# Kernel optimization log

Hardware: AMD Instinct MI355X
Metric: run time of the kernel (lower is better)

## Reference

```python
import jax, jax.numpy as jnp
import numpy as np

B, L, D, H = 2, 2048, 1024, 16
DH = D // H  # 64
SIGMA = float(np.sqrt(DH))  # sigma=None, learnable_sigma=False -> sqrt(d_head)


def setup_inputs() -> dict:
    key = jax.random.key(0)
    ks = jax.random.split(key, 5)
    x = jax.random.normal(ks[0], (B, L, D), dtype=jnp.float32)
    # causal visibility mask (1 = visible, 0 = masked), [B,1,L,L]
    mask = jnp.broadcast_to(jnp.tril(jnp.ones((L, L), jnp.int32))[None, None], (B, 1, L, L))
    scale = 0.02
    W_q = jax.random.normal(ks[1], (D, D), dtype=jnp.float32) * scale
    W_k = jax.random.normal(ks[2], (D, D), dtype=jnp.float32) * scale
    W_v = jax.random.normal(ks[3], (D, D), dtype=jnp.float32) * scale
    W_o = jax.random.normal(ks[4], (D, D), dtype=jnp.float32) * scale
    return {"x": x, "mask": mask, "W_q": W_q, "W_k": W_k, "W_v": W_v, "W_o": W_o}


def _split_heads(t):
    # [B,L,D] -> [B,H,L,DH]
    b, l, _ = t.shape
    return t.reshape(b, l, H, DH).transpose(0, 2, 1, 3)


def reference(x, mask, W_q, W_k, W_v, W_o):
    # nn.Linear(bias=False): y = x @ W.T
    Qh = _split_heads(x @ W_q.T)  # [B,H,L,DH]
    Kh = _split_heads(x @ W_k.T)
    Vh = _split_heads(x @ W_v.T)
    # RBF scores: -||q-k||^2 / (2 sigma^2)
    q_norm2 = jnp.sum(Qh * Qh, axis=-1, keepdims=True)          # [B,H,L,1]
    k_norm2 = jnp.sum(Kh * Kh, axis=-1)[..., None, :]            # [B,H,1,L]
    dot_qk = jnp.einsum('bhqd,bhkd->bhqk', Qh, Kh)               # [B,H,L,L]
    dist2 = q_norm2 + k_norm2 - 2.0 * dot_qk
    scores = -dist2 / (2.0 * SIGMA * SIGMA)
    scores = jnp.where(mask == 0, -jnp.inf, scores)
    attn = jax.nn.softmax(scores, axis=-1)
    Oh = jnp.einsum('bhqk,bhkd->bhqd', attn, Vh)                 # [B,H,L,DH]
    O = Oh.transpose(0, 2, 1, 3).reshape(B, L, D)
    return O @ W_o.T
```

## Files before the change

### kernel.cpp

```cpp
#include <hip/hip_runtime.h>

#define L_SEQ  2048
#define D_MODEL 1024
#define NH 16
#define DHEAD 64
#define BATCH 2

typedef __attribute__((ext_vector_type(8))) short bf16x8;
typedef __attribute__((ext_vector_type(4))) float f32x4;

__device__ inline ushort f2bf(float f) {
  unsigned int u = __builtin_bit_cast(unsigned int, f);
  return (ushort)((u + 0x7FFFu + ((u >> 16) & 1u)) >> 16);
}
__device__ inline float bf2f(ushort u) {
  return __builtin_bit_cast(float, (unsigned int)u << 16);
}

__device__ __forceinline__ void gload_lds16(const void* g, void* l) {
  __builtin_amdgcn_global_load_lds(
      (const __attribute__((address_space(1))) void*)g,
      (__attribute__((address_space(3))) void*)l, 16, 0, 0);
}

#define PROJ8 524288
#define WSZ8  131072
__global__ __launch_bounds__(256) void cvt_all(const float* __restrict__ x,
                                               const float* __restrict__ w0,
                                               const float* __restrict__ w1,
                                               const float* __restrict__ w2,
                                               const float* __restrict__ w3,
                                               ushort* __restrict__ xb,
                                               ushort* __restrict__ ob0,
                                               ushort* __restrict__ ob1,
                                               ushort* __restrict__ ob2,
                                               ushort* __restrict__ ob3) {
  const int gid = blockIdx.x * 256 + threadIdx.x;
  const float* in; ushort* out; int off;
  if (gid < PROJ8) { in = x; out = xb; off = gid; }
  else {
    const int j = gid - PROJ8;
    const int seg = j / WSZ8;
    off = j - seg * WSZ8;
    switch (seg) {
      case 0: in = w0; out = ob0; break;
      case 1: in = w1; out = ob1; break;
      case 2: in = w2; out = ob2; break;
      default: in = w3; out = ob3; break;
    }
  }
  const float4* p = (const float4*)in + (size_t)off * 2;
  const float4 a = p[0], b = p[1];
  ushort4 lo, hi;
  lo.x = f2bf(a.x); lo.y = f2bf(a.y); lo.z = f2bf(a.z); lo.w = f2bf(a.w);
  hi.x = f2bf(b.x); hi.y = f2bf(b.y); hi.z = f2bf(b.z); hi.w = f2bf(b.w);
  ((ushort4*)out)[(size_t)off * 2] = lo;
  ((ushort4*)out)[(size_t)off * 2 + 1] = hi;
}

__global__ __launch_bounds__(256) void gemm128(const ushort* __restrict__ A,
    const ushort* __restrict__ W0, const ushort* __restrict__ W1,
    const ushort* __restrict__ W2, ushort* __restrict__ o0,
    ushort* __restrict__ o1, ushort* __restrict__ o2,
    float* __restrict__ of, int fused) {
  __shared__ ushort As[2][128][32];
  __shared__ ushort Bs[2][128][32];
  const int tid = threadIdx.x;
  const int w = tid >> 6, l = tid & 63, lr = l & 15, lg = l >> 4;
  const int wr = w >> 1, wc = w & 1;

  const int cpx = gridDim.x >> 3;
  const int swz = (blockIdx.x & 7) * cpx + (blockIdx.x >> 3);
  const int NX = fused ? 24 : 8;
  const int ntile = swz % NX;
  const int m0 = (swz / NX) * 128;

  const ushort* W; ushort* ob; int mode;
  if (fused) {
    if (ntile < 8)       { W = W0; ob = o0; mode = 1; }
    else if (ntile < 16) { W = W1; ob = o1; mode = 1; }
    else                 { W = W2; ob = o2; mode = 2; }
  } else { W = W0; ob = o0; mode = 0; }
  const int n0 = (ntile & 7) * 128;

  const int srow = tid >> 2;
  const int skc_sw = (tid & 3) ^ (srow & 3);
  const ushort* Ag = A + (size_t)(m0 + srow) * D_MODEL + skc_sw * 8;
  const ushort* Wg = W + (size_t)(n0 + srow) * D_MODEL + skc_sw * 8;

#define STAGE(buf, k0)                                                      \
  {                                                                         \
    gload_lds16(Ag + (k0), &As[buf][0][0] + tid * 8);                       \
    gload_lds16(Ag + (size_t)64 * D_MODEL + (k0), &As[buf][0][0] + 2048 + tid * 8); \
    gload_lds16(Wg + (k0), &Bs[buf][0][0] + tid * 8);                       \
    gload_lds16(Wg + (size_t)64 * D_MODEL + (k0), &Bs[buf][0][0] + 2048 + tid * 8); \
  }

  STAGE(0, 0);

  f32x4 acc[4][4] = {};
  const int NT = D_MODEL / 32;
  for (int t = 0; t < NT; ++t) {
    const int cur = t & 1;
    if (t + 1 < NT) {
      STAGE(cur ^ 1, (t + 1) * 32);
      asm volatile("s_waitcnt vmcnt(4)" ::: "memory");
    } else {
      asm volatile("s_waitcnt vmcnt(0)" ::: "memory");
    }
    __builtin_amdgcn_s_barrier();

    bf16x8 af[4], bfv[4];
#pragma unroll
    for (int i = 0; i < 4; ++i)
      af[i] = *(const bf16x8*)&As[cur][wr * 64 + i * 16 + lr][(lg ^ (lr & 3)) * 8];
#pragma unroll
    for (int j = 0; j < 4; ++j)
      bfv[j] = *(const bf16x8*)&Bs[cur][wc * 64 + j * 16 + lr][(lg ^ (lr & 3)) * 8];
#pragma unroll
    for (int i = 0; i < 4; ++i)
#pragma unroll
      for (int j = 0; j < 4; ++j)
        acc[i][j] = __builtin_amdgcn_mfma_f32_16x16x32_bf16(af[i], bfv[j], acc[i][j], 0, 0, 0);
    __syncthreads();
  }

  if (mode == 0) {
#pragma unroll
    for (int i = 0; i < 4; ++i)
#pragma unroll
      for (int r = 0; r < 4; ++r) {
        const int m = m0 + wr * 64 + i * 16 + lg * 4 + r;
#pragma unroll
        for (int j = 0; j < 4; ++j)
          of[(size_t)m * D_MODEL + n0 + wc * 64 + j * 16 + lr] = acc[i][j][r];
      }
  } else if (mode == 1) {
    const int h = (ntile & 7) * 2 + wc;
#pragma unroll
    for (int i = 0; i < 4; ++i)
#pragma unroll
      for (int r = 0; r < 4; ++r) {
        const int m = m0 + wr * 64 + i * 16 + lg * 4 + r;
        const int b = m >> 11, ll = m & (L_SEQ - 1);
#pragma unroll
        for (int j = 0; j < 4; ++j)
          ob[((size_t)(b * NH + h) * L_SEQ + ll) * DHEAD + j * 16 + lr] = f2bf(acc[i][j][r]);
      }
  } else {
    const int h = (ntile & 7) * 2 + wc;
#pragma unroll
    for (int i = 0; i < 4; ++i) {
      const int mb = m0 + wr * 64 + i * 16 + lg * 4;
      const int b = mb >> 11, ll = mb & (L_SEQ - 1);
#pragma unroll
      for (int j = 0; j < 4; ++j) {
        ushort4 v;
        v.x = f2bf(acc[i][j][0]); v.y = f2bf(acc[i][j][1]);
        v.z = f2bf(acc[i][j][2]); v.w = f2bf(acc[i][j][3]);
        *(ushort4*)(ob + ((size_t)(b * NH + h) * DHEAD + j * 16 + lr) * L_SEQ + ll) = v;
      }
    }
  }
#undef STAGE
}

__global__ __launch_bounds__(256) void kn_bf16(const ushort* __restrict__ K,
                                               float* __restrict__ Kn) {
  const int i = blockIdx.x * 256 + threadIdx.x;
  const ushort4* p = (const ushort4*)(K + (size_t)i * DHEAD);
  float s = 0.f;
#pragma unroll
  for (int j = 0; j < 16; ++j) {
    const ushort4 v = p[j];
    const float a = bf2f(v.x), b = bf2f(v.y), c = bf2f(v.z), d = bf2f(v.w);
    s += a * a + b * b + c * c + d * d;
  }
  Kn[i] = s * 0.0078125f;
}

__global__ __launch_bounds__(512, 4) void attn_mfma3(const ushort* __restrict__ Q,
                                                     const ushort* __restrict__ K,
                                                     const ushort* __restrict__ Vt,
                                                     const float* __restrict__ Kexp,
                                                     ushort* __restrict__ Ob) {
  const int blk = blockIdx.x;
  const int qb = 15 - (blk >> 5);
  const int bh = blk & 31;
  const int tid = threadIdx.x;
  const int w = tid >> 6, l = tid & 63, lr = l & 15, lg = l >> 4;
  const int q0w = qb * 128 + w * 16;
  const int nt = 2 * qb + 2;
  const int tbw = q0w >> 6;

  __shared__ ushort Ks[2][64][64];
  __shared__ ushort Vs[2][64][64];
  __shared__ ushort P[8][16][70];

  const size_t ho = (size_t)bh * L_SEQ * DHEAD;
  const ushort* Qh = Q + ho;
  const ushort* Kh = K + ho;
  const ushort* Vh = Vt + ho;
  const float* KeB = Kexp + (size_t)bh * L_SEQ;

  const bf16x8 qf0 = *(const bf16x8*)(Qh + (size_t)(q0w + lr) * DHEAD + lg * 8);
  const bf16x8 qf1 = *(const bf16x8*)(Qh + (size_t)(q0w + lr) * DHEAD + 32 + lg * 8);

  const int srow = tid >> 3;
  const int scs = (tid & 7) ^ (srow & 7);
  const ushort* Kg = Kh + (size_t)srow * DHEAD + scs * 8;
  const ushort* Vg = Vh + (size_t)srow * L_SEQ + scs * 8;

  gload_lds16(Kg, &Ks[0][0][0] + tid * 8);
  gload_lds16(Vg, &Vs[0][0][0] + tid * 8);

  f32x4 oacc[4] = {};
  f32x4 lsacc = {};
  bf16x8 ones;
#pragma unroll
  for (int i = 0; i < 8; ++i) ones[i] = (short)0x3F80;

  for (int t = 0; t < nt; ++t) {
    const int cur = t & 1;
    if (t + 1 < nt) {
      const size_t kb2 = (size_t)(t + 1) * 64;
      gload_lds16(Kg + kb2 * DHEAD, &Ks[cur ^ 1][0][0] + tid * 8);
      gload_lds16(Vg + kb2, &Vs[cur ^ 1][0][0] + tid * 8);
      asm volatile("s_waitcnt vmcnt(2)" ::: "memory");
    } else {
      asm volatile("s_waitcnt vmcnt(0)" ::: "memory");
    }
    __builtin_amdgcn_s_barrier();

    const int kbase = t * 64;
    float ke[4];
#pragma unroll
    for (int nf = 0; nf < 4; ++nf) ke[nf] = KeB[kbase + nf * 16 + lr];
    const bool maskT = (t >= tbw);

    __builtin_amdgcn_s_setprio(1);
#pragma unroll
    for (int nf = 0; nf < 4; ++nf) {
      const int row = nf * 16 + lr;
      const bf16x8 kf0 = *(const bf16x8*)&Ks[cur][row][((lg) ^ (lr & 7)) * 8];
      const bf16x8 kf1 = *(const bf16x8*)&Ks[cur][row][((4 + lg) ^ (lr & 7)) * 8];
      f32x4 s = {0.f, 0.f, 0.f, 0.f};
      s = __builtin_amdgcn_mfma_f32_16x16x32_bf16(qf0, kf0, s, 0, 0, 0);
      s = __builtin_amdgcn_mfma_f32_16x16x32_bf16(qf1, kf1, s, 0, 0, 0);
      const int key = kbase + row;
      const float keh = ke[nf];
#pragma unroll
      for (int r = 0; r < 4; ++r) {
        float p = __expf(s[r] * 0.015625f - keh);
        if (maskT && key > q0w + lg * 4 + r) p = 0.f;
        P[w][lg * 4 + r][nf * 16 + lr] = f2bf(p);
      }
    }
    const bf16x8 p0 = *(const bf16x8*)&P[w][lr][lg * 8];
    const bf16x8 p1 = *(const bf16x8*)&P[w][lr][32 + lg * 8];
    lsacc = __builtin_amdgcn_mfma_f32_16x16x32_bf16(p0, ones, lsacc, 0, 0, 0);
    lsacc = __builtin_amdgcn_mfma_f32_16x16x32_bf16(p1, ones, lsacc, 0, 0, 0);
#pragma unroll
    for (int nf = 0; nf < 4; ++nf) {
      const int row = nf * 16 + lr;
      const bf16x8 vf0 = *(const bf16x8*)&Vs[cur][row][((lg) ^ (lr & 7)) * 8];
      const bf16x8 vf1 = *(const bf16x8*)&Vs[cur][row][((4 + lg) ^ (lr & 7)) * 8];
      oacc[nf] = __builtin_amdgcn_mfma_f32_16x16x32_bf16(p0, vf0, oacc[nf], 0, 0, 0);
      oacc[nf] = __builtin_amdgcn_mfma_f32_16x16x32_bf16(p1, vf1, oacc[nf], 0, 0, 0);
    }
    __builtin_amdgcn_s_setprio(0);
    __syncthreads();
  }

  const int b = bh >> 4, h = bh & 15;
#pragma unroll
  for (int r = 0; r < 4; ++r) {
    const float inv = 1.0f / lsacc[r];
    const int q = q0w + lg * 4 + r;
#pragma unroll
    for (int nf = 0; nf < 4; ++nf)
      Ob[((size_t)(b * L_SEQ + q)) * D_MODEL + h * DHEAD + nf * 16 + lr] =
          f2bf(oacc[nf][r] * inv);
  }
}

extern "C" void kernel_launch(void* const* d_in, const int* in_sizes, int n_in,
                              void* d_out, int out_size, void* d_ws, size_t ws_size,
                              hipStream_t stream) {
  const float* x  = (const float*)d_in[0];
  const float* Wq = (const float*)d_in[2];
  const float* Wk = (const float*)d_in[3];
  const float* Wv = (const float*)d_in[4];
  const float* Wo = (const float*)d_in[5];

  const size_t PROJ = (size_t)BATCH * L_SEQ * D_MODEL;
  const size_t WSZ  = (size_t)D_MODEL * D_MODEL;
  ushort* xb  = (ushort*)d_ws;
  ushort* Wqb = xb + PROJ;
  ushort* Wkb = Wqb + WSZ;
  ushort* Wvb = Wkb + WSZ;
  ushort* Wob = Wvb + WSZ;
  ushort* Qb  = Wob + WSZ;
  ushort* Kb  = Qb + PROJ;
  ushort* Vtb = Kb + PROJ;
  ushort* Obf = Vtb + PROJ;
  float*  Kn  = (float*)(Obf + PROJ);

  cvt_all<<<(PROJ8 + 4 * WSZ8) / 256, 256, 0, stream>>>(x, Wq, Wk, Wv, Wo,
                                                        xb, Wqb, Wkb, Wvb, Wob);
  gemm128<<<768, 256, 0, stream>>>(xb, Wqb, Wkb, Wvb, Qb, Kb, Vtb, nullptr, 1);
  kn_bf16<<<BATCH * NH * L_SEQ / 256, 256, 0, stream>>>(Kb, Kn);
  attn_mfma3<<<BATCH * NH * (L_SEQ / 128), 512, 0, stream>>>(Qb, Kb, Vtb, Kn, Obf);
  gemm128<<<256, 256, 0, stream>>>(Obf, Wob, nullptr, nullptr, Obf, nullptr,
                                   nullptr, (float*)d_out, 0);
}
```

Measured before the change: 146.9 us.

## Replace QKV projection GEMM with 256x256-tile 8-wave phased pipeline kernel

Adds a new QKV projection kernel that uses 256x256 output tiles with 8 waves, K-steps of 64, and double-buffered LDS. Global-to-LDS loads are split across four compute phases so each MFMA phase overlaps one staging load, with setprio raised around the MFMA bursts. The larger tile raises arithmetic intensity per LDS byte, but the grid drops from 768 blocks to 192 on a 256-CU part, which risks underfilling the device. The output GEMM is simplified to a single mode, and one trailing __syncthreads in the attention loop becomes a raw s_barrier.

```diff
diff --git a/kernel.cpp b/kernel.cpp
--- a/kernel.cpp
+++ b/kernel.cpp
@@ -58,11 +58,149 @@
   ((ushort4*)out)[(size_t)off * 2 + 1] = hi;
 }
 
+__global__ __launch_bounds__(512, 2) void gemm8p(const ushort* __restrict__ A,
+    const ushort* __restrict__ W0, const ushort* __restrict__ W1,
+    const ushort* __restrict__ W2, ushort* __restrict__ Qb,
+    ushort* __restrict__ Kb, ushort* __restrict__ Vtb) {
+  __shared__ ushort As[2][2][128][64];
+  __shared__ ushort Bs[2][2][128][64];
+  const int tid = threadIdx.x;
+  const int wid = tid >> 6, l = tid & 63, lr = l & 15, lg = l >> 4;
+  const int wr = wid >> 2, wc = wid & 3;
+
+  const int bid = blockIdx.x;
+  const int swz = (bid & 7) * 24 + (bid >> 3);
+  const int mt = swz / 12, nt_ = swz % 12;
+  const int m0g = mt * 256;
+  const ushort* W = (nt_ < 4) ? W0 : (nt_ < 8) ? W1 : W2;
+  ushort* outQK = (nt_ < 4) ? Qb : Kb;
+  const int mode2 = (nt_ >= 8);
+  const int ncol0 = (nt_ & 3) * 256;
+
+  const int srow = tid >> 3;
+  const int schunk = (tid & 7) ^ (srow & 7);
+  const ushort* Ag = A + (size_t)(m0g + srow) * D_MODEL + schunk * 8;
+  const ushort* Wg = W + (size_t)(ncol0 + srow) * D_MODEL + schunk * 8;
+  ushort* AsL = &As[0][0][0][0] + tid * 8;
+  ushort* BsL = &Bs[0][0][0][0] + tid * 8;
+
+#define STG_A(sl, h, T2)                                                        \
+  {                                                                             \
+    gload_lds16(Ag + (size_t)((h) * 128) * D_MODEL + (T2) * 64,                 \
+                AsL + (sl) * 16384 + (h) * 8192);                               \
+    gload_lds16(Ag + (size_t)((h) * 128 + 64) * D_MODEL + (T2) * 64,            \
+                AsL + (sl) * 16384 + (h) * 8192 + 4096);                        \
+  }
+#define STG_B(sl, h, T2)                                                        \
+  {                                                                             \
+    gload_lds16(Wg + (size_t)((h) * 128) * D_MODEL + (T2) * 64,                 \
+                BsL + (sl) * 16384 + (h) * 8192);                               \
+    gload_lds16(Wg + (size_t)((h) * 128 + 64) * D_MODEL + (T2) * 64,            \
+                BsL + (sl) * 16384 + (h) * 8192 + 4096);                        \
+  }
+
+  STG_A(0, 0, 0); STG_A(0, 1, 0); STG_B(0, 0, 0); STG_B(0, 1, 0);
+
+  f32x4 acc[8][4] = {};
+  bf16x8 bfr[4][2];
+  const int NT = D_MODEL / 64;
+
+#define PHASE(q)                                                                \
+  {                                                                             \
+    bf16x8 af[2][2];                                                            \
+    _Pragma("unroll") for (int m2 = 0; m2 < 2; ++m2)                            \
+      _Pragma("unroll") for (int kk = 0; kk < 2; ++kk)                          \
+        af[m2][kk] = *(const bf16x8*)&As[s][wr][((q) * 2 + m2) * 16 + lr]       \
+                                           [((kk * 4 + lg) ^ (lr & 7)) * 8];    \
+    if (T + 1 < NT) {                                                           \
+      if ((q) == 1)      { STG_A(s ^ 1, 1, T + 1); }                            \
+      else if ((q) == 2) { STG_B(s ^ 1, 0, T + 1); }                            \
+      else               { STG_B(s ^ 1, 1, T + 1); }                            \
+    }                                                                           \
+    __builtin_amdgcn_s_barrier();                                               \
+    __builtin_amdgcn_s_setprio(1);                                              \
+    _Pragma("unroll") for (int m2 = 0; m2 < 2; ++m2)                            \
+      _Pragma("unroll") for (int kk = 0; kk < 2; ++kk)                          \
+        _Pragma("unroll") for (int n = 0; n < 4; ++n)                           \
+          acc[(q) * 2 + m2][n] = __builtin_amdgcn_mfma_f32_16x16x32_bf16(       \
+              af[m2][kk], bfr[n][kk], acc[(q) * 2 + m2][n], 0, 0, 0);           \
+    __builtin_amdgcn_s_setprio(0);                                              \
+    __builtin_amdgcn_s_barrier();                                               \
+  }
+
+  for (int T = 0; T < NT; ++T) {
+    const int s = T & 1;
+    {
+      if (T + 1 < NT) {
+        STG_A(s ^ 1, 0, T + 1);
+        asm volatile("s_waitcnt vmcnt(2)" ::: "memory");
+      } else {
+        asm volatile("s_waitcnt vmcnt(0)" ::: "memory");
+      }
+      __builtin_amdgcn_s_barrier();
+#pragma unroll
+      for (int n = 0; n < 4; ++n)
+#pragma unroll
+        for (int kk = 0; kk < 2; ++kk)
+          bfr[n][kk] = *(const bf16x8*)&Bs[s][wc >> 1][(wc & 1) * 64 + n * 16 + lr]
+                                          [((kk * 4 + lg) ^ (lr & 7)) * 8];
+      bf16x8 af[2][2];
+#pragma unroll
+      for (int m2 = 0; m2 < 2; ++m2)
+#pragma unroll
+        for (int kk = 0; kk < 2; ++kk)
+          af[m2][kk] = *(const bf16x8*)&As[s][wr][m2 * 16 + lr]
+                                          [((kk * 4 + lg) ^ (lr & 7)) * 8];
+      __builtin_amdgcn_s_setprio(1);
+#pragma unroll
+      for (int m2 = 0; m2 < 2; ++m2)
+#pragma unroll
+        for (int kk = 0; kk < 2; ++kk)
+#pragma unroll
+          for (int n = 0; n < 4; ++n)
+            acc[m2][n] = __builtin_amdgcn_mfma_f32_16x16x32_bf16(
+                af[m2][kk], bfr[n][kk], acc[m2][n], 0, 0, 0);
+      __builtin_amdgcn_s_setprio(0);
+      __builtin_amdgcn_s_barrier();
+    }
+    PHASE(1)
+    PHASE(2)
+    PHASE(3)
+  }
+#undef PHASE
+#undef STG_A
+#undef STG_B
+
+  const int h = (nt_ & 3) * 4 + wc;
+  if (!mode2) {
+#pragma unroll
+    for (int m = 0; m < 8; ++m)
+#pragma unroll
+      for (int r = 0; r < 4; ++r) {
+        const int grow = m0g + wr * 128 + m * 16 + lg * 4 + r;
+        const int b = grow >> 11, ll = grow & (L_SEQ - 1);
+        ushort* dst = outQK + ((size_t)(b * NH + h) * L_SEQ + ll) * DHEAD;
+#pragma unroll
+        for (int n = 0; n < 4; ++n) dst[n * 16 + lr] = f2bf(acc[m][n][r]);
+      }
+  } else {
+#pragma unroll
+    for (int m = 0; m < 8; ++m) {
+      const int grow0 = m0g + wr * 128 + m * 16 + lg * 4;
+      const int b = grow0 >> 11, ll = grow0 & (L_SEQ - 1);
+#pragma unroll
+      for (int n = 0; n < 4; ++n) {
+        ushort4 v;
+        v.x = f2bf(acc[m][n][0]); v.y = f2bf(acc[m][n][1]);
+        v.z = f2bf(acc[m][n][2]); v.w = f2bf(acc[m][n][3]);
+        *(ushort4*)(Vtb + ((size_t)(b * NH + h) * DHEAD + n * 16 + lr) * L_SEQ + ll) = v;
+      }
+    }
+  }
+}
+
 __global__ __launch_bounds__(256) void gemm128(const ushort* __restrict__ A,
-    const ushort* __restrict__ W0, const ushort* __restrict__ W1,
-    const ushort* __restrict__ W2, ushort* __restrict__ o0,
-    ushort* __restrict__ o1, ushort* __restrict__ o2,
-    float* __restrict__ of, int fused) {
+    const ushort* __restrict__ W0, float* __restrict__ of) {
   __shared__ ushort As[2][128][32];
   __shared__ ushort Bs[2][128][32];
   const int tid = threadIdx.x;
@@ -71,22 +209,14 @@
 
   const int cpx = gridDim.x >> 3;
   const int swz = (blockIdx.x & 7) * cpx + (blockIdx.x >> 3);
-  const int NX = fused ? 24 : 8;
-  const int ntile = swz % NX;
-  const int m0 = (swz / NX) * 128;
-
-  const ushort* W; ushort* ob; int mode;
-  if (fused) {
-    if (ntile < 8)       { W = W0; ob = o0; mode = 1; }
-    else if (ntile < 16) { W = W1; ob = o1; mode = 1; }
-    else                 { W = W2; ob = o2; mode = 2; }
-  } else { W = W0; ob = o0; mode = 0; }
-  const int n0 = (ntile & 7) * 128;
+  const int ntile = swz % 8;
+  const int m0 = (swz / 8) * 128;
+  const int n0 = ntile * 128;
 
   const int srow = tid >> 2;
   const int skc_sw = (tid & 3) ^ (srow & 3);
   const ushort* Ag = A + (size_t)(m0 + srow) * D_MODEL + skc_sw * 8;
-  const ushort* Wg = W + (size_t)(n0 + srow) * D_MODEL + skc_sw * 8;
+  const ushort* Wg = W0 + (size_t)(n0 + srow) * D_MODEL + skc_sw * 8;
 
 #define STAGE(buf, k0)                                                      \
   {                                                                         \
@@ -124,45 +254,17 @@
         acc[i][j] = __builtin_amdgcn_mfma_f32_16x16x32_bf16(af[i], bfv[j], acc[i][j], 0, 0, 0);
     __syncthreads();
   }
-
-  if (mode == 0) {
-#pragma unroll
-    for (int i = 0; i < 4; ++i)
-#pragma unroll
-      for (int r = 0; r < 4; ++r) {
-        const int m = m0 + wr * 64 + i * 16 + lg * 4 + r;
-#pragma unroll
-        for (int j = 0; j < 4; ++j)
-          of[(size_t)m * D_MODEL + n0 + wc * 64 + j * 16 + lr] = acc[i][j][r];
-      }
-  } else if (mode == 1) {
-    const int h = (ntile & 7) * 2 + wc;
-#pragma unroll
-    for (int i = 0; i < 4; ++i)
-#pragma unroll
-      for (int r = 0; r < 4; ++r) {
-        const int m = m0 + wr * 64 + i * 16 + lg * 4 + r;
-        const int b = m >> 11, ll = m & (L_SEQ - 1);
-#pragma unroll
-        for (int j = 0; j < 4; ++j)
-          ob[((size_t)(b * NH + h) * L_SEQ + ll) * DHEAD + j * 16 + lr] = f2bf(acc[i][j][r]);
-      }
-  } else {
-    const int h = (ntile & 7) * 2 + wc;
-#pragma unroll
-    for (int i = 0; i < 4; ++i) {
-      const int mb = m0 + wr * 64 + i * 16 + lg * 4;
-      const int b = mb >> 11, ll = mb & (L_SEQ - 1);
-#pragma unroll
-      for (int j = 0; j < 4; ++j) {
-        ushort4 v;
-        v.x = f2bf(acc[i][j][0]); v.y = f2bf(acc[i][j][1]);
-        v.z = f2bf(acc[i][j][2]); v.w = f2bf(acc[i][j][3]);
-        *(ushort4*)(ob + ((size_t)(b * NH + h) * DHEAD + j * 16 + lr) * L_SEQ + ll) = v;
-      }
-    }
-  }
 #undef STAGE
+
+#pragma unroll
+  for (int i = 0; i < 4; ++i)
+#pragma unroll
+    for (int r = 0; r < 4; ++r) {
+      const int m = m0 + wr * 64 + i * 16 + lg * 4 + r;
+#pragma unroll
+      for (int j = 0; j < 4; ++j)
+        of[(size_t)m * D_MODEL + n0 + wc * 64 + j * 16 + lr] = acc[i][j][r];
+    }
 }
 
 __global__ __launch_bounds__(256) void kn_bf16(const ushort* __restrict__ K,
@@ -269,7 +371,7 @@
       oacc[nf] = __builtin_amdgcn_mfma_f32_16x16x32_bf16(p1, vf1, oacc[nf], 0, 0, 0);
     }
     __builtin_amdgcn_s_setprio(0);
-    __syncthreads();
+    __builtin_amdgcn_s_barrier();
   }
 
   const int b = bh >> 4, h = bh & 15;
@@ -308,9 +410,8 @@
 
   cvt_all<<<(PROJ8 + 4 * WSZ8) / 256, 256, 0, stream>>>(x, Wq, Wk, Wv, Wo,
                                                         xb, Wqb, Wkb, Wvb, Wob);
-  gemm128<<<768, 256, 0, stream>>>(xb, Wqb, Wkb, Wvb, Qb, Kb, Vtb, nullptr, 1);
+  gemm8p<<<192, 512, 0, stream>>>(xb, Wqb, Wkb, Wvb, Qb, Kb, Vtb);
   kn_bf16<<<BATCH * NH * L_SEQ / 256, 256, 0, stream>>>(Kb, Kn);
   attn_mfma3<<<BATCH * NH * (L_SEQ / 128), 512, 0, stream>>>(Qb, Kb, Vtb, Kn, Obf);
-  gemm128<<<256, 256, 0, stream>>>(Obf, Wob, nullptr, nullptr, Obf, nullptr,
-                                   nullptr, (float*)d_out, 0);
-}
+  gemm128<<<256, 256, 0, stream>>>(Obf, Wob, (float*)d_out);
+}
```

Measured after the change: 133.9 us. -8.8%, faster.
